# Optimization experiments

Measured on AMD Instinct MI355X. Metric: run time of the kernel, lower is better.

Reference implementation:

```python
import jax, jax.numpy as jnp
import numpy as np

B, S, DIM = 2, 2048, 2048
H, KVH = 16, 8
HD = DIM // H            # 128
WIN = 512                # sliding window size
GLOB = 64                # global tokens
NEG = -1000000000.0


def _alibi_slopes(n):
    cp2 = 2.0 ** jnp.floor(jnp.log2(jnp.float32(n)))
    base = 2.0 ** (-(2.0 ** (-(jnp.log2(cp2) - 3.0))))
    powers = jnp.arange(1, 1 + n, dtype=jnp.float32)
    return jnp.power(base, powers)  # [n]


def _rope_tables(head_dim, seq_len, dtype=jnp.float32, base=10000.0):
    half = head_dim // 2
    freqs = 1.0 / base ** (jnp.arange(0, half, dtype=dtype) / half)
    t = jnp.arange(seq_len, dtype=dtype)
    f = jnp.outer(t, freqs)                       # [S, half]
    return jnp.sin(f)[None, None], jnp.cos(f)[None, None]  # [1,1,S,half]


def _rotary(x, sin, cos):
    # x: [b,h,s,d]; nonstandard rotation per source module
    x1, x2 = jnp.split(x, 2, axis=-1)
    return jnp.concatenate([x1 * cos - x2 * sin, x1 * sin + x2 * cos], axis=-1)


def _window_mask(seq_len):
    # Faithful to create_sliding_window_mask: 0.0 inside window / global rows+cols, -1e9 elsewhere
    i = jnp.arange(seq_len)[:, None]
    j = jnp.arange(seq_len)[None, :]
    m = jnp.where(jnp.abs(i - j) <= WIN // 2, 0.0, NEG)
    m = jnp.where((i < GLOB) | (j < GLOB), 0.0, m)
    return m  # [S, S] float


def setup_inputs() -> dict:
    key = jax.random.key(0)
    k1, k2, k3, k4 = jax.random.split(key, 4)
    x = jax.random.normal(k1, (B, S, DIM), dtype=jnp.float32)
    Wq = jax.random.normal(k2, (DIM, DIM), dtype=jnp.float32) * 0.02
    Wkv = jax.random.normal(k3, (DIM, 2 * KVH * HD), dtype=jnp.float32) * 0.02
    Wo = jax.random.normal(k4, (DIM, DIM), dtype=jnp.float32) * 0.02
    bo = jnp.zeros((DIM,), dtype=jnp.float32)
    return {"x": x, "Wq": Wq, "Wkv": Wkv, "Wo": Wo, "bo": bo}


def reference(x, Wq, Wkv, Wo, bo):
    b, s, dim = x.shape
    # token-complexity gating on queries
    complexity = jax.nn.sigmoid(jnp.sum(jnp.abs(x), axis=-1, keepdims=True))  # [b,s,1]
    q = jnp.dot(x * complexity, Wq)       # [b,s,dim]
    kv = jnp.dot(x, Wkv)                  # [b,s,2*kv_dim]
    k, v = jnp.split(kv, 2, axis=-1)

    q = q.reshape(b, s, H, HD).transpose(0, 2, 1, 3)      # [b,H,s,d]
    k = k.reshape(b, s, KVH, HD).transpose(0, 2, 1, 3)    # [b,KVH,s,d]
    v = v.reshape(b, s, KVH, HD).transpose(0, 2, 1, 3)

    sin, cos = _rope_tables(HD, s, dtype=x.dtype)
    q = _rotary(q, sin, cos)
    k = _rotary(k, sin, cos)

    r = H // KVH
    k = jnp.repeat(k, r, axis=1)   # 'b h s d -> b (h r) s d'
    v = jnp.repeat(v, r, axis=1)

    scale = 1.0 / jnp.sqrt(jnp.float32(HD)).astype(x.dtype)
    qk = jnp.einsum('bhid,bhjd->bhij', q, k) * scale      # [b,H,s,s]

    # ALiBi bias
    slopes = _alibi_slopes(H)                             # [H]
    pos = jnp.arange(s)
    dist = -jnp.abs(pos[:, None] - pos[None, :]).astype(jnp.float32)  # [s,s]
    qk = qk + slopes[:, None, None] * dist                # broadcast over batch

    # Faithful to source: jnp.where(float_mask, qk, NEG) treats nonzero (-1e9,
    # i.e. OUTSIDE window) as True -> keeps qk; zero (inside window) -> NEG.
    m = _window_mask(s)
    qk = jnp.where(m != 0.0, qk, NEG)

    attn = jax.nn.softmax(qk, axis=-1)
    out = jnp.einsum('bhij,bhjd->bhid', attn, v)          # [b,H,s,d]
    out = out.transpose(0, 2, 1, 3).reshape(b, s, dim)
    out = jnp.dot(out, Wo) + bo
    return out
```

## Files before the change

kernel.cpp:

```cpp
#include <hip/hip_runtime.h>

#define DEVI static __device__ __forceinline__

typedef __attribute__((ext_vector_type(8))) short short8;
typedef __attribute__((ext_vector_type(4))) short short4v;
typedef __attribute__((ext_vector_type(4))) float f32x4;

DEVI float bf2f(short u) {
  union { unsigned u32; float f; } c;
  c.u32 = ((unsigned)(unsigned short)u) << 16;
  return c.f;
}
DEVI short f2bf(float f) {
  union { float f; unsigned u32; } c; c.f = f;
  unsigned x = c.u32;
  unsigned r = (x + 0x7FFFu + ((x >> 16) & 1u)) >> 16;
  return (short)(unsigned short)r;
}
DEVI float ex2(float x) {
  float r;
  asm("v_exp_f32 %0, %1" : "=v"(r) : "v"(x));
  return r;
}
DEVI unsigned cvtpk(float lo, float hi) {
  unsigned r;
  asm("v_cvt_pk_bf16_f32 %0, %1, %2" : "=v"(r) : "v"(lo), "v"(hi));
  return r;
}

DEVI void gload16(const void* g, void* l) {
  __builtin_amdgcn_global_load_lds(
      (__attribute__((address_space(1))) void*)(g),
      (__attribute__((address_space(3))) void*)(l), 16, 0, 0);
}

#define LOG2E 1.4426950408889634f
#define QSCALE 0.1275174470974102f

__global__ void prep_x_kernel(const float* __restrict__ x,
                              short* __restrict__ xq, short* __restrict__ xb) {
  int row = blockIdx.x, t = threadIdx.x;
  const float4* xr = (const float4*)(x + (size_t)row * 2048);
  float4 v0 = xr[t], v1 = xr[t + 256];
  float s = fabsf(v0.x) + fabsf(v0.y) + fabsf(v0.z) + fabsf(v0.w)
          + fabsf(v1.x) + fabsf(v1.y) + fabsf(v1.z) + fabsf(v1.w);
#pragma unroll
  for (int m = 1; m < 64; m <<= 1) s += __shfl_xor(s, m, 64);
  __shared__ float red[4];
  if ((t & 63) == 0) red[t >> 6] = s;
  __syncthreads();
  float tot = red[0] + red[1] + red[2] + red[3];
  float sc = 1.0f / (1.0f + expf(-tot));
  short4v q0, q1, b0, b1;
  q0[0] = f2bf(v0.x * sc); q0[1] = f2bf(v0.y * sc); q0[2] = f2bf(v0.z * sc); q0[3] = f2bf(v0.w * sc);
  q1[0] = f2bf(v1.x * sc); q1[1] = f2bf(v1.y * sc); q1[2] = f2bf(v1.z * sc); q1[3] = f2bf(v1.w * sc);
  b0[0] = f2bf(v0.x); b0[1] = f2bf(v0.y); b0[2] = f2bf(v0.z); b0[3] = f2bf(v0.w);
  b1[0] = f2bf(v1.x); b1[1] = f2bf(v1.y); b1[2] = f2bf(v1.z); b1[3] = f2bf(v1.w);
  size_t base = (size_t)row * 512;
  ((short4v*)xq)[base + t]       = q0;
  ((short4v*)xq)[base + t + 256] = q1;
  ((short4v*)xb)[base + t]       = b0;
  ((short4v*)xb)[base + t + 256] = b1;
}

__global__ void sincos_kernel(float* __restrict__ tsin, float* __restrict__ tcos) {
  int idx = blockIdx.x * 256 + threadIdx.x;
  int d = idx >> 11, s = idx & 2047;
  float freq = powf(10000.0f, -(float)d / 64.0f);
  float f = (float)s * freq;
  tsin[idx] = sinf(f);
  tcos[idx] = cosf(f);
}

__global__ void wtrans_kernel(const float* __restrict__ W, short* __restrict__ WT) {
  __shared__ __align__(16) short tile[64][68];
  int n0 = blockIdx.x * 64, k0 = blockIdx.y * 64;
  int t = threadIdx.x;
  int tr = t >> 4, tc = t & 15;
#pragma unroll
  for (int p = 0; p < 4; ++p) {
    int r = p * 16 + tr;
    int c = tc * 4;
    float4 v = *(const float4*)&W[(size_t)(k0 + r) * 2048 + n0 + c];
    tile[c + 0][r] = f2bf(v.x);
    tile[c + 1][r] = f2bf(v.y);
    tile[c + 2][r] = f2bf(v.z);
    tile[c + 3][r] = f2bf(v.w);
  }
  __syncthreads();
#pragma unroll
  for (int p = 0; p < 4; ++p) {
    int n = p * 16 + tr;
    int c = tc * 4;
    *(short4v*)&WT[(size_t)(n0 + n) * 2048 + k0 + c] = *(const short4v*)&tile[n][c];
  }
}

template<int EPI>
__launch_bounds__(256, 2)
__global__ void gemm_kernel(const short* __restrict__ A, const short* __restrict__ BT,
                            void* __restrict__ Cout, short* __restrict__ aux,
                            const float* __restrict__ bias,
                            const float* __restrict__ tsin, const float* __restrict__ tcos,
                            int M, int N, int K) {
  __shared__ __align__(16) short As[128 * 32];
  __shared__ __align__(16) short Bs[128 * 32];
  const int tid = threadIdx.x;
  const int wid = tid >> 6, lane = tid & 63;
  const int nb = gridDim.x * gridDim.y;
  const int orig = blockIdx.y * gridDim.x + blockIdx.x;
  const int swz = (orig & 7) * (nb >> 3) + (orig >> 3);
  const int m0 = (swz / gridDim.x) * 128, n0 = (swz % gridDim.x) * 128;
  const int l15 = lane & 15, l4 = lane >> 4;
  f32x4 acc[2][8] = {};
  for (int k0 = 0; k0 < K; k0 += 32) {
#pragma unroll
    for (int p = 0; p < 2; ++p) {
      int chunk = wid + p * 4;
      int off = chunk * 1024 + lane * 16;
      int row = off >> 6;
      int cole = (off & 63) >> 1;
      gload16(A + (size_t)(m0 + row) * K + k0 + cole, &As[chunk * 512]);
      gload16(BT + (size_t)(n0 + row) * K + k0 + cole, &Bs[chunk * 512]);
    }
    __syncthreads();
    short8 af[2], bfr[8];
#pragma unroll
    for (int i = 0; i < 2; ++i)
      af[i] = *(const short8*)&As[(wid * 32 + i * 16 + l15) * 32 + l4 * 8];
#pragma unroll
    for (int i = 0; i < 8; ++i)
      bfr[i] = *(const short8*)&Bs[(i * 16 + l15) * 32 + l4 * 8];
#pragma unroll
    for (int mi = 0; mi < 2; ++mi)
#pragma unroll
      for (int ni = 0; ni < 8; ++ni)
        acc[mi][ni] = __builtin_amdgcn_mfma_f32_16x16x32_bf16(af[mi], bfr[ni], acc[mi][ni], 0, 0, 0);
    __syncthreads();
  }

  if (EPI == 0) {
#pragma unroll
    for (int mi = 0; mi < 2; ++mi) {
#pragma unroll
      for (int ni = 0; ni < 8; ++ni) {
        int col = n0 + ni * 16 + l15;
        float badd = bias[col];
#pragma unroll
        for (int r = 0; r < 4; ++r) {
          int row = m0 + wid * 32 + mi * 16 + l4 * 4 + r;
          ((float*)Cout)[(size_t)row * N + col] = acc[mi][ni][r] + badd;
        }
      }
    }
  } else if (EPI == 1) {
    const int h = n0 >> 7;
    const int b = m0 >> 11;
    const int sb = (m0 & 2047) + wid * 32;
    short* qr = (short*)Cout;
    const size_t obase = ((size_t)(b * 16 + h) * 2048 + sb) * 128;
#pragma unroll
    for (int mi = 0; mi < 2; ++mi) {
      int srel = sb + mi * 16 + l4 * 4;
#pragma unroll
      for (int ni = 0; ni < 4; ++ni) {
        int d = ni * 16 + l15;
        float4 sn = *(const float4*)&tsin[d * 2048 + srel];
        float4 cs = *(const float4*)&tcos[d * 2048 + srel];
#pragma unroll
        for (int r = 0; r < 4; ++r) {
          float x1 = acc[mi][ni][r], x2 = acc[mi][ni + 4][r];
          float snr = (&sn.x)[r], csr = (&cs.x)[r];
          size_t ro = obase + (size_t)(mi * 16 + l4 * 4 + r) * 128;
          qr[ro + d]      = f2bf((x1 * csr - x2 * snr) * QSCALE);
          qr[ro + d + 64] = f2bf((x1 * snr + x2 * csr) * QSCALE);
        }
      }
    }
  } else {
    const int b = m0 >> 11;
    const int sb = (m0 & 2047) + wid * 32;
    if (n0 < 1024) {
      const int kvh = n0 >> 7;
      short* kr = (short*)Cout;
      const size_t obase = ((size_t)(b * 8 + kvh) * 2048 + sb) * 128;
#pragma unroll
      for (int mi = 0; mi < 2; ++mi) {
        int srel = sb + mi * 16 + l4 * 4;
#pragma unroll
        for (int ni = 0; ni < 4; ++ni) {
          int d = ni * 16 + l15;
          float4 sn = *(const float4*)&tsin[d * 2048 + srel];
          float4 cs = *(const float4*)&tcos[d * 2048 + srel];
#pragma unroll
          for (int r = 0; r < 4; ++r) {
            float x1 = acc[mi][ni][r], x2 = acc[mi][ni + 4][r];
            float snr = (&sn.x)[r], csr = (&cs.x)[r];
            size_t ro = obase + (size_t)(mi * 16 + l4 * 4 + r) * 128;
            kr[ro + d]      = f2bf(x1 * csr - x2 * snr);
            kr[ro + d + 64] = f2bf(x1 * snr + x2 * csr);
          }
        }
      }
    } else {
      const int kvh = (n0 - 1024) >> 7;
      short* vt = aux;
      const size_t vb = (size_t)(b * 8 + kvh) * 128;
#pragma unroll
      for (int mi = 0; mi < 2; ++mi) {
        int srel = sb + mi * 16 + l4 * 4;
#pragma unroll
        for (int ni = 0; ni < 8; ++ni) {
          int d = ni * 16 + l15;
          uint2 w;
          w.x = cvtpk(acc[mi][ni][0], acc[mi][ni][1]);
          w.y = cvtpk(acc[mi][ni][2], acc[mi][ni][3]);
          *(uint2*)&vt[(vb + d) * 2048 + srel] = w;
        }
      }
    }
  }
}

__launch_bounds__(512, 4)
__global__ void attn_kernel(const short* __restrict__ qr, const short* __restrict__ kr,
                            const short* __restrict__ vt, short* __restrict__ ob) {
  __shared__ __align__(16) short Ks[2][64 * 128];
  __shared__ __align__(16) short Vs[2][128 * 64];
  __shared__ __align__(16) short PL[8][16 * 64];
  const int tid = threadIdx.x;
  const int wid = tid >> 6, lane = tid & 63;
  const int l15 = lane & 15, l4 = lane >> 4;
  const int sw7 = l15 & 7;
  const int l4h = l4 >> 1, l4l = l4 & 1;
  const int qt = blockIdx.x, h = blockIdx.y, b = blockIdx.z;
  const int kh = h >> 1;
  const int qb = qt * 128;
  const int q0 = qb + wid * 16;
  const float slope2 = exp2f(-0.5f * (float)(h + 1)) * LOG2E;
  const size_t qbase = ((size_t)(b * 16 + h) * 2048 + q0) * 128;
  const size_t kbase = ((size_t)(b * 8 + kh) * 2048) * 128;
  const size_t vbase = ((size_t)(b * 8 + kh) * 128) * 2048;
  short* pl = PL[wid];

  short8 aq[4];
#pragma unroll
  for (int kk = 0; kk < 4; ++kk)
    aq[kk] = *(const short8*)&qr[qbase + (size_t)l15 * 128 + kk * 32 + l4 * 8];

  f32x4 o[8] = {};
  float m_run = -1e30f, l_run = 0.0f;
  const int iq = q0 + l15;

  int lo0, n0t, lo1, n1t;
  if (qt == 0)      { lo0 = 0;   n0t = 32;          lo1 = 0; n1t = 0; }
  else if (qt == 1) { lo0 = 384; n0t = 26;          lo1 = 0; n1t = 0; }
  else {
    lo0 = 64;        n0t = 2 * qt - 3;
    lo1 = qb + 256;  n1t = (28 - 2 * qt > 0) ? (28 - 2 * qt) : 0;
  }
  const int nt = n0t + n1t;
  auto KV0 = [&](int i) { return i < n0t ? lo0 + i * 64 : lo1 + (i - n0t) * 64; };

  auto STAGE = [&](int bi, int kv0) {
#pragma unroll
    for (int i2 = 0; i2 < 2; ++i2) {
      int cid = i2 * 512 + tid;
      int krow = cid >> 4, kch = cid & 15;
      gload16(kr + kbase + (size_t)(kv0 + krow) * 128 + ((kch ^ (krow & 7)) * 8),
              &Ks[bi][cid * 8]);
    }
#pragma unroll
    for (int i2 = 0; i2 < 2; ++i2) {
      int cid = i2 * 512 + tid;
      int vrow = cid >> 3, vch = cid & 7;
      gload16(vt + vbase + (size_t)vrow * 2048 + kv0 + ((vch ^ (vrow & 7)) * 8),
              &Vs[bi][cid * 8]);
    }
  };

  STAGE(0, KV0(0));
  __syncthreads();
  int cur = 0;

  for (int it = 0; it < nt; ++it) {
    const int kv0 = KV0(it);
    if (it + 1 < nt) STAGE(cur ^ 1, KV0(it + 1));

    int mode;
    if (q0 + 15 < 64 || kv0 == 0) mode = 3;
    else if (kv0 <= q0 - 320)     mode = 1;
    else if (kv0 >= q0 + 272)     mode = 2;
    else                          mode = 0;

    if (mode != 3) {
      f32x4 sc[4];
#pragma unroll
      for (int jj = 0; jj < 4; ++jj) sc[jj] = (f32x4){0.f, 0.f, 0.f, 0.f};
      __builtin_amdgcn_s_setprio(1);
#pragma unroll
      for (int kk = 0; kk < 4; ++kk) {
#pragma unroll
        for (int jj = 0; jj < 4; ++jj) {
          short8 bk = *(const short8*)&Ks[cur][(jj * 16 + l15) * 128 + (((kk * 4 + l4) ^ sw7) * 8)];
          sc[jj] = __builtin_amdgcn_mfma_f32_16x16x32_bf16(bk, aq[kk], sc[jj], 0, 0, 0);
        }
      }
      __builtin_amdgcn_s_setprio(0);
      float pm = -1e30f;
      const float dbase = (float)(iq - kv0 - l4 * 4);
      if (mode == 0) {
#pragma unroll
        for (int jj = 0; jj < 4; ++jj) {
          float dj = dbase - 16.0f * jj;
#pragma unroll
          for (int r = 0; r < 4; ++r) {
            float d = dj - (float)r;
            float ad = fabsf(d);
            float v = fmaf(-slope2, ad, sc[jj][r]);
            v = (ad > 256.0f) ? v : -1e9f;
            sc[jj][r] = v;
            pm = fmaxf(pm, v);
          }
        }
      } else {
        const float sl = (mode == 1) ? -slope2 : slope2;
#pragma unroll
        for (int jj = 0; jj < 4; ++jj) {
          float dj = dbase - 16.0f * jj;
#pragma unroll
          for (int r = 0; r < 4; ++r) {
            float v = fmaf(sl, dj - (float)r, sc[jj][r]);
            sc[jj][r] = v;
            pm = fmaxf(pm, v);
          }
        }
      }
      pm = fmaxf(pm, __shfl_xor(pm, 16, 64));
      pm = fmaxf(pm, __shfl_xor(pm, 32, 64));
      if (!__all(pm <= m_run + 8.0f)) {
        float mn = fmaxf(m_run, pm);
        float corr = ex2(m_run - mn);
        l_run *= corr;
#pragma unroll
        for (int dn = 0; dn < 8; ++dn)
#pragma unroll
          for (int r = 0; r < 4; ++r) o[dn][r] *= corr;
        m_run = mn;
      }
      float psum = 0.0f;
#pragma unroll
      for (int jj = 0; jj < 4; ++jj) {
        float p0 = ex2(sc[jj][0] - m_run);
        float p1 = ex2(sc[jj][1] - m_run);
        float p2 = ex2(sc[jj][2] - m_run);
        float p3 = ex2(sc[jj][3] - m_run);
        psum += (p0 + p1) + (p2 + p3);
        uint2 w; w.x = cvtpk(p0, p1); w.y = cvtpk(p2, p3);
        int ad = l15 * 64 + (((jj * 2 + l4h) ^ sw7) * 8) + l4l * 4;
        *(uint2*)&pl[ad] = w;
      }
      psum += __shfl_xor(psum, 16, 64);
      psum += __shfl_xor(psum, 32, 64);
      l_run += psum;
      asm volatile("s_waitcnt lgkmcnt(0)" ::: "memory");
      __builtin_amdgcn_sched_barrier(0);
      __builtin_amdgcn_s_setprio(1);
#pragma unroll
      for (int c = 0; c < 2; ++c) {
        short8 pa = *(const short8*)&pl[l15 * 64 + (((c * 4 + l4) ^ sw7) * 8)];
#pragma unroll
        for (int dn = 0; dn < 8; ++dn) {
          short8 bv = *(const short8*)&Vs[cur][(dn * 16 + l15) * 64 + (((c * 4 + l4) ^ sw7) * 8)];
          o[dn] = __builtin_amdgcn_mfma_f32_16x16x32_bf16(bv, pa, o[dn], 0, 0, 0);
        }
      }
      __builtin_amdgcn_s_setprio(0);
    } else {
      float pm = -1e9f;
      if (!__all(pm <= m_run + 8.0f)) {
        float mn = fmaxf(m_run, pm);
        float corr = ex2(m_run - mn);
        l_run *= corr;
#pragma unroll
        for (int dn = 0; dn < 8; ++dn)
#pragma unroll
          for (int r = 0; r < 4; ++r) o[dn][r] *= corr;
        m_run = mn;
      }
      float pu = ex2(-1e9f - m_run);
      l_run += 64.0f * pu;
      unsigned uu = cvtpk(pu, pu);
      short8 pa;
      ((unsigned*)&pa)[0] = uu; ((unsigned*)&pa)[1] = uu;
      ((unsigned*)&pa)[2] = uu; ((unsigned*)&pa)[3] = uu;
      __builtin_amdgcn_s_setprio(1);
#pragma unroll
      for (int c = 0; c < 2; ++c) {
#pragma unroll
        for (int dn = 0; dn < 8; ++dn) {
          short8 bv = *(const short8*)&Vs[cur][(dn * 16 + l15) * 64 + (((c * 4 + l4) ^ sw7) * 8)];
          o[dn] = __builtin_amdgcn_mfma_f32_16x16x32_bf16(bv, pa, o[dn], 0, 0, 0);
        }
      }
      __builtin_amdgcn_s_setprio(0);
    }
    __syncthreads();
    cur ^= 1;
  }

  float inv = 1.0f / l_run;
  size_t rbase = ((size_t)(b * 2048 + iq) * 16 + h) * 128;
#pragma unroll
  for (int dn = 0; dn < 8; ++dn) {
    uint2 w;
    w.x = cvtpk(o[dn][0] * inv, o[dn][1] * inv);
    w.y = cvtpk(o[dn][2] * inv, o[dn][3] * inv);
    *(uint2*)&ob[rbase + dn * 16 + l4 * 4] = w;
  }
}

extern "C" void kernel_launch(void* const* d_in, const int* in_sizes, int n_in,
                              void* d_out, int out_size, void* d_ws, size_t ws_size,
                              hipStream_t stream) {
  const float* x   = (const float*)d_in[0];
  const float* Wq  = (const float*)d_in[1];
  const float* Wkv = (const float*)d_in[2];
  const float* Wo  = (const float*)d_in[3];
  const float* bo  = (const float*)d_in[4];
  float* out = (float*)d_out;

  char* ws = (char*)d_ws;
  size_t off = 0;
  auto alloc = [&](size_t bytes) -> void* {
    void* p = ws + off;
    off += (bytes + 255) & ~(size_t)255;
    return p;
  };
  float* tsin  = (float*)alloc(64 * 2048 * 4);
  float* tcos  = (float*)alloc(64 * 2048 * 4);
  short* WqT   = (short*)alloc((size_t)2048 * 2048 * 2);
  short* WkvT  = (short*)alloc((size_t)2048 * 2048 * 2);
  short* WoT   = (short*)alloc((size_t)2048 * 2048 * 2);
  short* xq    = (short*)alloc((size_t)4096 * 2048 * 2);
  short* xb    = (short*)alloc((size_t)4096 * 2048 * 2);
  short* qr    = (short*)alloc((size_t)2 * 16 * 2048 * 128 * 2);
  short* kr    = (short*)alloc((size_t)2 * 8 * 2048 * 128 * 2);
  short* vt    = (short*)alloc((size_t)2 * 8 * 2048 * 128 * 2);
  short* ob    = xq;

  prep_x_kernel<<<4096, 256, 0, stream>>>(x, xq, xb);
  sincos_kernel<<<512, 256, 0, stream>>>(tsin, tcos);
  wtrans_kernel<<<dim3(32, 32), 256, 0, stream>>>(Wq, WqT);
  wtrans_kernel<<<dim3(32, 32), 256, 0, stream>>>(Wkv, WkvT);
  wtrans_kernel<<<dim3(32, 32), 256, 0, stream>>>(Wo, WoT);
  gemm_kernel<1><<<dim3(16, 32), 256, 0, stream>>>(xq, WqT, qr, nullptr, nullptr, tsin, tcos, 4096, 2048, 2048);
  gemm_kernel<2><<<dim3(16, 32), 256, 0, stream>>>(xb, WkvT, kr, vt, nullptr, tsin, tcos, 4096, 2048, 2048);
  attn_kernel<<<dim3(16, 16, 2), 512, 0, stream>>>(qr, kr, vt, ob);
  gemm_kernel<0><<<dim3(16, 32), 256, 0, stream>>>(ob, WoT, (void*)out, nullptr, bo, nullptr, nullptr, 4096, 2048, 2048);
  (void)in_sizes; (void)n_in; (void)out_size; (void)ws_size;
}
```

Measured before the change: 260.6 us.

## Rewrite GEMM as double-buffered 128x256 tiles with swizzled LDS, fuse weight transposes

The GEMM kernel moves from a single-buffered 128x128 tile with K-step 32 and 4 waves to a 128x256 tile with K-step 64, 8 waves, double-buffered LDS with XOR-swizzled layout, and explicit waitcnt/barrier pipelining that splits the B tile into two halves to overlap loads with MFMA. The three weight-transpose launches are merged into one grid. The attention kernel's block order is also remapped with a swizzle for better cache locality. The larger LDS footprint (96KB per block) and 512 threads may limit occupancy, and the hand-tuned vmcnt counts are fragile.

```diff
diff --git a/kernel.cpp b/kernel.cpp
--- a/kernel.cpp
+++ b/kernel.cpp
@@ -72,8 +72,13 @@
   tcos[idx] = cosf(f);
 }
 
-__global__ void wtrans_kernel(const float* __restrict__ W, short* __restrict__ WT) {
+__global__ void wtrans_kernel(const float* __restrict__ W0, const float* __restrict__ W1,
+                              const float* __restrict__ W2,
+                              short* __restrict__ T0, short* __restrict__ T1,
+                              short* __restrict__ T2) {
   __shared__ __align__(16) short tile[64][68];
+  const float* W = blockIdx.z == 0 ? W0 : (blockIdx.z == 1 ? W1 : W2);
+  short* WT      = blockIdx.z == 0 ? T0 : (blockIdx.z == 1 ? T1 : T2);
   int n0 = blockIdx.x * 64, k0 = blockIdx.y * 64;
   int t = threadIdx.x;
   int tr = t >> 4, tc = t & 15;
@@ -97,124 +102,178 @@
 }
 
 template<int EPI>
-__launch_bounds__(256, 2)
+__launch_bounds__(512, 2)
 __global__ void gemm_kernel(const short* __restrict__ A, const short* __restrict__ BT,
                             void* __restrict__ Cout, short* __restrict__ aux,
                             const float* __restrict__ bias,
                             const float* __restrict__ tsin, const float* __restrict__ tcos,
                             int M, int N, int K) {
-  __shared__ __align__(16) short As[128 * 32];
-  __shared__ __align__(16) short Bs[128 * 32];
+  __shared__ __align__(16) short As[2][128 * 64];
+  __shared__ __align__(16) short Bs[2][2][128 * 64];
   const int tid = threadIdx.x;
   const int wid = tid >> 6, lane = tid & 63;
   const int nb = gridDim.x * gridDim.y;
   const int orig = blockIdx.y * gridDim.x + blockIdx.x;
   const int swz = (orig & 7) * (nb >> 3) + (orig >> 3);
-  const int m0 = (swz / gridDim.x) * 128, n0 = (swz % gridDim.x) * 128;
+  const int m0 = (swz / gridDim.x) * 128, n0 = (swz % gridDim.x) * 256;
+  const int wr = wid >> 2, wc = wid & 3;
   const int l15 = lane & 15, l4 = lane >> 4;
-  f32x4 acc[2][8] = {};
-  for (int k0 = 0; k0 < K; k0 += 32) {
+  const int T = K >> 6;
+
+  auto STAGE_A = [&](int bi, int t) {
 #pragma unroll
     for (int p = 0; p < 2; ++p) {
-      int chunk = wid + p * 4;
-      int off = chunk * 1024 + lane * 16;
-      int row = off >> 6;
-      int cole = (off & 63) >> 1;
-      gload16(A + (size_t)(m0 + row) * K + k0 + cole, &As[chunk * 512]);
-      gload16(BT + (size_t)(n0 + row) * K + k0 + cole, &Bs[chunk * 512]);
-    }
-    __syncthreads();
-    short8 af[2], bfr[8];
-#pragma unroll
-    for (int i = 0; i < 2; ++i)
-      af[i] = *(const short8*)&As[(wid * 32 + i * 16 + l15) * 32 + l4 * 8];
-#pragma unroll
-    for (int i = 0; i < 8; ++i)
-      bfr[i] = *(const short8*)&Bs[(i * 16 + l15) * 32 + l4 * 8];
-#pragma unroll
-    for (int mi = 0; mi < 2; ++mi)
-#pragma unroll
-      for (int ni = 0; ni < 8; ++ni)
-        acc[mi][ni] = __builtin_amdgcn_mfma_f32_16x16x32_bf16(af[mi], bfr[ni], acc[mi][ni], 0, 0, 0);
-    __syncthreads();
-  }
-
+      int cid = p * 512 + tid;
+      int row = cid >> 3, ch = cid & 7;
+      gload16(A + (size_t)(m0 + row) * K + t * 64 + ((ch ^ (row & 7)) * 8),
+              &As[bi][cid * 8]);
+    }
+  };
+  auto STAGE_B = [&](int bi, int h, int t) {
+#pragma unroll
+    for (int p = 0; p < 2; ++p) {
+      int cid = p * 512 + tid;
+      int row = cid >> 3, ch = cid & 7;
+      gload16(BT + (size_t)(n0 + h * 128 + row) * K + t * 64 + ((ch ^ (row & 7)) * 8),
+              &Bs[bi][h][cid * 8]);
+    }
+  };
+
+  f32x4 acc[4][4] = {};
+  STAGE_A(0, 0); STAGE_B(0, 0, 0); STAGE_B(0, 1, 0);
+  asm volatile("s_waitcnt vmcnt(2)" ::: "memory");
+  __builtin_amdgcn_s_barrier();
+
+  for (int t = 0; t < T; ++t) {
+    const int cur = t & 1;
+    short8 af[4][2], bf[2][2];
+    if (t + 1 < T) { STAGE_A(cur ^ 1, t + 1); STAGE_B(cur ^ 1, 0, t + 1); }
+#pragma unroll
+    for (int mi = 0; mi < 4; ++mi) {
+      int ra = wr * 64 + mi * 16 + l15;
+#pragma unroll
+      for (int kk = 0; kk < 2; ++kk)
+        af[mi][kk] = *(const short8*)&As[cur][ra * 64 + (((kk * 4 + l4) ^ (ra & 7)) * 8)];
+    }
+#pragma unroll
+    for (int ni = 0; ni < 2; ++ni) {
+      int rb = ni * 64 + wc * 16 + l15;
+#pragma unroll
+      for (int kk = 0; kk < 2; ++kk)
+        bf[ni][kk] = *(const short8*)&Bs[cur][0][rb * 64 + (((kk * 4 + l4) ^ (rb & 7)) * 8)];
+    }
+    if (t + 1 < T) asm volatile("s_waitcnt vmcnt(4)" ::: "memory");
+    else           asm volatile("s_waitcnt vmcnt(0)" ::: "memory");
+    __builtin_amdgcn_s_barrier();
+    asm volatile("s_waitcnt lgkmcnt(0)" ::: "memory");
+    __builtin_amdgcn_sched_barrier(0);
+    __builtin_amdgcn_s_setprio(1);
+#pragma unroll
+    for (int kk = 0; kk < 2; ++kk)
+#pragma unroll
+      for (int mi = 0; mi < 4; ++mi)
+#pragma unroll
+        for (int ni = 0; ni < 2; ++ni)
+          acc[mi][ni] = __builtin_amdgcn_mfma_f32_16x16x32_bf16(af[mi][kk], bf[ni][kk], acc[mi][ni], 0, 0, 0);
+    __builtin_amdgcn_s_setprio(0);
+    __builtin_amdgcn_s_barrier();
+    if (t + 1 < T) STAGE_B(cur ^ 1, 1, t + 1);
+#pragma unroll
+    for (int ni = 0; ni < 2; ++ni) {
+      int rb = ni * 64 + wc * 16 + l15;
+#pragma unroll
+      for (int kk = 0; kk < 2; ++kk)
+        bf[ni][kk] = *(const short8*)&Bs[cur][1][rb * 64 + (((kk * 4 + l4) ^ (rb & 7)) * 8)];
+    }
+    if (t + 1 < T) asm volatile("s_waitcnt vmcnt(2)" ::: "memory");
+    __builtin_amdgcn_s_barrier();
+    asm volatile("s_waitcnt lgkmcnt(0)" ::: "memory");
+    __builtin_amdgcn_sched_barrier(0);
+    __builtin_amdgcn_s_setprio(1);
+#pragma unroll
+    for (int kk = 0; kk < 2; ++kk)
+#pragma unroll
+      for (int mi = 0; mi < 4; ++mi)
+#pragma unroll
+        for (int ni = 0; ni < 2; ++ni)
+          acc[mi][ni + 2] = __builtin_amdgcn_mfma_f32_16x16x32_bf16(af[mi][kk], bf[ni][kk], acc[mi][ni + 2], 0, 0, 0);
+    __builtin_amdgcn_s_setprio(0);
+    __builtin_amdgcn_s_barrier();
+  }
+
+  const int b = m0 >> 11;
+  const int sb = (m0 & 2047) + wr * 64;
+  const int d0 = wc * 16 + l15;
   if (EPI == 0) {
 #pragma unroll
-    for (int mi = 0; mi < 2; ++mi) {
-#pragma unroll
-      for (int ni = 0; ni < 8; ++ni) {
-        int col = n0 + ni * 16 + l15;
-        float badd = bias[col];
+    for (int j = 0; j < 4; ++j) {
+      int col = n0 + (j >> 1) * 128 + (j & 1) * 64 + d0;
+      float badd = bias[col];
+#pragma unroll
+      for (int mi = 0; mi < 4; ++mi) {
 #pragma unroll
         for (int r = 0; r < 4; ++r) {
-          int row = m0 + wid * 32 + mi * 16 + l4 * 4 + r;
-          ((float*)Cout)[(size_t)row * N + col] = acc[mi][ni][r] + badd;
+          int row = m0 + wr * 64 + mi * 16 + l4 * 4 + r;
+          ((float*)Cout)[(size_t)row * N + col] = acc[mi][j][r] + badd;
         }
       }
     }
   } else if (EPI == 1) {
-    const int h = n0 >> 7;
-    const int b = m0 >> 11;
-    const int sb = (m0 & 2047) + wid * 32;
     short* qr = (short*)Cout;
-    const size_t obase = ((size_t)(b * 16 + h) * 2048 + sb) * 128;
-#pragma unroll
-    for (int mi = 0; mi < 2; ++mi) {
-      int srel = sb + mi * 16 + l4 * 4;
-#pragma unroll
-      for (int ni = 0; ni < 4; ++ni) {
-        int d = ni * 16 + l15;
-        float4 sn = *(const float4*)&tsin[d * 2048 + srel];
-        float4 cs = *(const float4*)&tcos[d * 2048 + srel];
+#pragma unroll
+    for (int p = 0; p < 2; ++p) {
+      int h = (n0 >> 7) + p;
+      size_t obase = ((size_t)(b * 16 + h) * 2048 + sb) * 128;
+#pragma unroll
+      for (int mi = 0; mi < 4; ++mi) {
+        int srel = sb + mi * 16 + l4 * 4;
+        float4 sn = *(const float4*)&tsin[d0 * 2048 + srel];
+        float4 cs = *(const float4*)&tcos[d0 * 2048 + srel];
 #pragma unroll
         for (int r = 0; r < 4; ++r) {
-          float x1 = acc[mi][ni][r], x2 = acc[mi][ni + 4][r];
+          float x1 = acc[mi][2 * p][r], x2 = acc[mi][2 * p + 1][r];
           float snr = (&sn.x)[r], csr = (&cs.x)[r];
           size_t ro = obase + (size_t)(mi * 16 + l4 * 4 + r) * 128;
-          qr[ro + d]      = f2bf((x1 * csr - x2 * snr) * QSCALE);
-          qr[ro + d + 64] = f2bf((x1 * snr + x2 * csr) * QSCALE);
+          qr[ro + d0]      = f2bf((x1 * csr - x2 * snr) * QSCALE);
+          qr[ro + d0 + 64] = f2bf((x1 * snr + x2 * csr) * QSCALE);
         }
       }
     }
   } else {
-    const int b = m0 >> 11;
-    const int sb = (m0 & 2047) + wid * 32;
     if (n0 < 1024) {
-      const int kvh = n0 >> 7;
       short* kr = (short*)Cout;
-      const size_t obase = ((size_t)(b * 8 + kvh) * 2048 + sb) * 128;
-#pragma unroll
-      for (int mi = 0; mi < 2; ++mi) {
-        int srel = sb + mi * 16 + l4 * 4;
-#pragma unroll
-        for (int ni = 0; ni < 4; ++ni) {
-          int d = ni * 16 + l15;
-          float4 sn = *(const float4*)&tsin[d * 2048 + srel];
-          float4 cs = *(const float4*)&tcos[d * 2048 + srel];
+#pragma unroll
+      for (int p = 0; p < 2; ++p) {
+        int kvh = (n0 >> 7) + p;
+        size_t obase = ((size_t)(b * 8 + kvh) * 2048 + sb) * 128;
+#pragma unroll
+        for (int mi = 0; mi < 4; ++mi) {
+          int srel = sb + mi * 16 + l4 * 4;
+          float4 sn = *(const float4*)&tsin[d0 * 2048 + srel];
+          float4 cs = *(const float4*)&tcos[d0 * 2048 + srel];
 #pragma unroll
           for (int r = 0; r < 4; ++r) {
-            float x1 = acc[mi][ni][r], x2 = acc[mi][ni + 4][r];
+            float x1 = acc[mi][2 * p][r], x2 = acc[mi][2 * p + 1][r];
             float snr = (&sn.x)[r], csr = (&cs.x)[r];
             size_t ro = obase + (size_t)(mi * 16 + l4 * 4 + r) * 128;
-            kr[ro + d]      = f2bf(x1 * csr - x2 * snr);
-            kr[ro + d + 64] = f2bf(x1 * snr + x2 * csr);
+            kr[ro + d0]      = f2bf(x1 * csr - x2 * snr);
+            kr[ro + d0 + 64] = f2bf(x1 * snr + x2 * csr);
           }
         }
       }
     } else {
-      const int kvh = (n0 - 1024) >> 7;
       short* vt = aux;
-      const size_t vb = (size_t)(b * 8 + kvh) * 128;
-#pragma unroll
-      for (int mi = 0; mi < 2; ++mi) {
-        int srel = sb + mi * 16 + l4 * 4;
-#pragma unroll
-        for (int ni = 0; ni < 8; ++ni) {
-          int d = ni * 16 + l15;
+#pragma unroll
+      for (int j = 0; j < 4; ++j) {
+        int kvh = ((n0 - 1024) >> 7) + (j >> 1);
+        int d = (j & 1) * 64 + d0;
+        size_t vb = (size_t)(b * 8 + kvh) * 128;
+#pragma unroll
+        for (int mi = 0; mi < 4; ++mi) {
+          int srel = sb + mi * 16 + l4 * 4;
           uint2 w;
-          w.x = cvtpk(acc[mi][ni][0], acc[mi][ni][1]);
-          w.y = cvtpk(acc[mi][ni][2], acc[mi][ni][3]);
+          w.x = cvtpk(acc[mi][j][0], acc[mi][j][1]);
+          w.y = cvtpk(acc[mi][j][2], acc[mi][j][3]);
           *(uint2*)&vt[(vb + d) * 2048 + srel] = w;
         }
       }
@@ -233,7 +292,9 @@
   const int l15 = lane & 15, l4 = lane >> 4;
   const int sw7 = l15 & 7;
   const int l4h = l4 >> 1, l4l = l4 & 1;
-  const int qt = blockIdx.x, h = blockIdx.y, b = blockIdx.z;
+  const int f = blockIdx.x + (blockIdx.y << 4) + (blockIdx.z << 8);
+  const int swb = (f & 7) * 64 + (f >> 3);
+  const int qt = swb & 15, h = (swb >> 4) & 15, b = swb >> 8;
   const int kh = h >> 1;
   const int qb = qt * 128;
   const int q0 = qb + wid * 16;
@@ -451,12 +512,10 @@
 
   prep_x_kernel<<<4096, 256, 0, stream>>>(x, xq, xb);
   sincos_kernel<<<512, 256, 0, stream>>>(tsin, tcos);
-  wtrans_kernel<<<dim3(32, 32), 256, 0, stream>>>(Wq, WqT);
-  wtrans_kernel<<<dim3(32, 32), 256, 0, stream>>>(Wkv, WkvT);
-  wtrans_kernel<<<dim3(32, 32), 256, 0, stream>>>(Wo, WoT);
-  gemm_kernel<1><<<dim3(16, 32), 256, 0, stream>>>(xq, WqT, qr, nullptr, nullptr, tsin, tcos, 4096, 2048, 2048);
-  gemm_kernel<2><<<dim3(16, 32), 256, 0, stream>>>(xb, WkvT, kr, vt, nullptr, tsin, tcos, 4096, 2048, 2048);
+  wtrans_kernel<<<dim3(32, 32, 3), 256, 0, stream>>>(Wq, Wkv, Wo, WqT, WkvT, WoT);
+  gemm_kernel<1><<<dim3(8, 32), 512, 0, stream>>>(xq, WqT, qr, nullptr, nullptr, tsin, tcos, 4096, 2048, 2048);
+  gemm_kernel<2><<<dim3(8, 32), 512, 0, stream>>>(xb, WkvT, kr, vt, nullptr, tsin, tcos, 4096, 2048, 2048);
   attn_kernel<<<dim3(16, 16, 2), 512, 0, stream>>>(qr, kr, vt, ob);
-  gemm_kernel<0><<<dim3(16, 32), 256, 0, stream>>>(ob, WoT, (void*)out, nullptr, bo, nullptr, nullptr, 4096, 2048, 2048);
+  gemm_kernel<0><<<dim3(8, 32), 512, 0, stream>>>(ob, WoT, (void*)out, nullptr, bo, nullptr, nullptr, 4096, 2048, 2048);
   (void)in_sizes; (void)n_in; (void)out_size; (void)ws_size;
 }
```

Result: slower. 302.5 us (+16.1%).
